# Optimization experiments

Measured on AMD Instinct MI355X. Metric: run time of the kernel, lower is better.

## Reference

```python
import jax, jax.numpy as jnp
import numpy as np

EMPTY = -1  # sentinel for empty (vertex, region) slots, as in the TF layer


def setup_inputs() -> dict:
    key = jax.random.key(0)
    m, vertices, regions = 128, 2048, 32
    # values in [-1, vertices): -1 marks an empty slot, otherwise a vertex id
    mapping = jax.random.randint(key, (m, vertices, regions), EMPTY, vertices, dtype=jnp.int32)
    return {"mapping": mapping}


def reference(mapping):
    """Faithful JAX version of Graph2Col.call.

    TF's tf.where(mask) emits coordinates of True entries in row-major order
    with a data-dependent row count. For jit-compatibility we emit a
    fixed-size [m*V*R, ...] result where valid entries come first (same
    row-major order as tf.where) and padding rows are filled with -1.
    """
    m, V, R = mapping.shape
    total = m * V * R
    flat_map = mapping.reshape(-1)                 # [total]
    # row index is never -1, so the reduce_all mask is simply mapping != -1
    flat_mask = flat_map != EMPTY                  # [total] bool

    # stable stream compaction: valid entries first, preserving row-major order
    order = jnp.argsort(~flat_mask)                # stable sort -> tf.where ordering
    valid = flat_mask[order]                       # [total] bool

    rows = order // (V * R)
    rem = order % (V * R)
    verts = rem // R
    regs = rem % R

    # column_indices: coordinates of non-empty slots (tf.where returns int64)
    column_indices = jnp.stack([rows, verts, regs], axis=-1).astype(jnp.int64)  # [total, 3]
    # nodes_indices: (batch_row, vertex_id) gathered at those coordinates (int32)
    nodes_indices = jnp.stack([rows.astype(jnp.int32), flat_map[order]], axis=-1)  # [total, 2]

    column_indices = jnp.where(valid[:, None], column_indices, jnp.int64(EMPTY))
    nodes_indices = jnp.where(valid[:, None], nodes_indices, jnp.int32(EMPTY))
    return nodes_indices, column_indices
```

## Files before the change

kernel.cpp:

```cpp
#include <hip/hip_runtime.h>


#define EMPTY_V (-1)

constexpr int M_DIM = 128;
constexpr int V_DIM = 2048;
constexpr int R_DIM = 32;
constexpr int TOTAL = M_DIM * V_DIM * R_DIM;
constexpr int BLOCK = 256;
constexpr int CHUNK = 8192;
constexpr int NB = TOTAL / CHUNK;
constexpr int SUBT = CHUNK / (BLOCK * 4);
constexpr int NWAVE = BLOCK / 64;
constexpr int STAGE = BLOCK * 4;

__global__ __launch_bounds__(BLOCK) void k_count(const int* __restrict__ in,
                                                 int* __restrict__ counts) {
    const int b = blockIdx.x;
    const int tid = threadIdx.x;
    const int4* p = (const int4*)(in + (size_t)b * CHUNK);
    int c = 0;
#pragma unroll
    for (int s = 0; s < SUBT; ++s) {
        int4 v = p[s * BLOCK + tid];
        c += (v.x != EMPTY_V) + (v.y != EMPTY_V) + (v.z != EMPTY_V) + (v.w != EMPTY_V);
    }
    for (int d = 32; d > 0; d >>= 1) c += __shfl_down(c, d, 64);
    __shared__ int ws[NWAVE];
    const int lane = tid & 63, wid = tid >> 6;
    if (lane == 0) ws[wid] = c;
    __syncthreads();
    if (tid == 0) {
        int t = 0;
        for (int w = 0; w < NWAVE; ++w) t += ws[w];
        counts[b] = t;
    }
}

__global__ __launch_bounds__(BLOCK) void k_scatter(const int* __restrict__ in,
                                                   const int* __restrict__ counts,
                                                   int* __restrict__ out_nodes,
                                                   int* __restrict__ out_cols) {
    const int b = blockIdx.x;
    const int tid = threadIdx.x;
    const int lane = tid & 63, wid = tid >> 6;
    const unsigned long long below = lane ? ((~0ull) >> (64 - lane)) : 0ull;

    __shared__ int red[2 * NWAVE];
    {
        const int4 c4 = ((const int4*)counts)[tid];
        const int idx0 = tid * 4;
        const int cs[4] = {c4.x, c4.y, c4.z, c4.w};
        int pa = 0, ta = 0;
#pragma unroll
        for (int j = 0; j < 4; ++j) {
            ta += cs[j];
            if (idx0 + j < b) pa += cs[j];
        }
        for (int d = 32; d > 0; d >>= 1) {
            pa += __shfl_down(pa, d, 64);
            ta += __shfl_down(ta, d, 64);
        }
        if (lane == 0) { red[wid] = pa; red[NWAVE + wid] = ta; }
    }
    __syncthreads();
    int running = 0, tv = 0;
    for (int w = 0; w < NWAVE; ++w) { running += red[w]; tv += red[NWAVE + w]; }

    __shared__ int wsum[NWAVE];
    __shared__ int s_val[STAGE];
    __shared__ int s_pos[STAGE];
    const int row = b >> 3;
    const int4* p = (const int4*)(in + (size_t)b * CHUNK);
#pragma unroll 1
    for (int s = 0; s < SUBT; ++s) {
        const int4 v = p[s * BLOCK + tid];
        const int f0 = (v.x != EMPTY_V), f1 = (v.y != EMPTY_V);
        const int f2 = (v.z != EMPTY_V), f3 = (v.w != EMPTY_V);
        const unsigned long long b0 = __ballot(f0), b1 = __ballot(f1);
        const unsigned long long b2 = __ballot(f2), b3 = __ballot(f3);
        const int pre = __popcll(b0 & below) + __popcll(b1 & below) +
                        __popcll(b2 & below) + __popcll(b3 & below);
        const int wtot = __popcll(b0) + __popcll(b1) + __popcll(b2) + __popcll(b3);
        if (lane == 0) wsum[wid] = wtot;
        __syncthreads();
        int woff = 0, cnt = 0;
        for (int w = 0; w < NWAVE; ++w) {
            const int x = wsum[w];
            cnt += x;
            if (w < wid) woff += x;
        }
        int lp = woff + pre;
        const int rem0 = ((b & 7) << 13) + (s << 10) + (tid << 2);
        const int vals[4] = {v.x, v.y, v.z, v.w};
        const int fl[4] = {f0, f1, f2, f3};
#pragma unroll
        for (int j = 0; j < 4; ++j) {
            if (fl[j]) { s_val[lp] = vals[j]; s_pos[lp] = rem0 + j; ++lp; }
        }
        __syncthreads();

        {
            int2* b2p = (int2*)out_nodes + running;
            const int head = ((running & 1) && cnt > 0) ? 1 : 0;
            if (head && tid == 0) b2p[0] = make_int2(row, s_val[0]);
            const int nPairs = (cnt - head) >> 1;
            int4* b4p = (int4*)(b2p + head);
            for (int k = tid; k < nPairs; k += BLOCK) {
                const int e = head + 2 * k;
                b4p[k] = make_int4(row, s_val[e], row, s_val[e + 1]);
            }
            if (((cnt - head) & 1) && tid == BLOCK - 1)
                b2p[cnt - 1] = make_int2(row, s_val[cnt - 1]);
        }
        {
            int* cd = out_cols + 3 * (size_t)running;
            const int cdw = 3 * cnt;
            const int mis = (3 * running) & 3;
            int peel = mis ? (4 - mis) : 0;
            if (peel > cdw) peel = cdw;
            if (tid < peel) {
                const int ld = tid;
                const int e = ld / 3, r = ld - 3 * e;
                int vv = row;
                if (r) { const int pp = s_pos[e]; vv = (r == 1) ? (pp >> 5) : (pp & 31); }
                cd[ld] = vv;
            }
            const int body = (cdw - peel) >> 2;
            int4* c4p = (int4*)(cd + peel);
            for (int k = tid; k < body; k += BLOCK) {
                const int ld0 = peel + 4 * k;
                int vv[4];
#pragma unroll
                for (int i = 0; i < 4; ++i) {
                    const int ld = ld0 + i;
                    const int e = ld / 3, r = ld - 3 * e;
                    int x = row;
                    if (r) { const int pp = s_pos[e]; x = (r == 1) ? (pp >> 5) : (pp & 31); }
                    vv[i] = x;
                }
                c4p[k] = make_int4(vv[0], vv[1], vv[2], vv[3]);
            }
            const int tails = cdw - peel - 4 * body;
            if (tid < tails) {
                const int ld = peel + 4 * body + tid;
                const int e = ld / 3, r = ld - 3 * e;
                int vv = row;
                if (r) { const int pp = s_pos[e]; vv = (r == 1) ? (pp >> 5) : (pp & 31); }
                cd[ld] = vv;
            }
        }
        running += cnt;
        __syncthreads();
    }

    for (int pos = tv + b * BLOCK + tid; pos < TOTAL; pos += NB * BLOCK) {
        out_nodes[2 * pos]     = EMPTY_V;
        out_nodes[2 * pos + 1] = EMPTY_V;
        out_cols[3 * pos]      = EMPTY_V;
        out_cols[3 * pos + 1]  = EMPTY_V;
        out_cols[3 * pos + 2]  = EMPTY_V;
    }
}

extern "C" void kernel_launch(void* const* d_in, const int* in_sizes, int n_in,
                              void* d_out, int out_size, void* d_ws, size_t ws_size,
                              hipStream_t stream) {
    const int* in = (const int*)d_in[0];
    int* out = (int*)d_out;
    int* out_nodes = out;
    int* out_cols = out + 2 * (size_t)TOTAL;
    int* counts = (int*)d_ws;

    k_count<<<NB, BLOCK, 0, stream>>>(in, counts);
    k_scatter<<<NB, BLOCK, 0, stream>>>(in, counts, out_nodes, out_cols);
}
```

Before: 192.0 us.

## Fuse count and scatter into single-pass decoupled look-back scan kernel

Replaces the two-kernel count-then-scatter compaction with one kernel. Each block keeps its input chunk in registers, publishes its aggregate and inclusive prefix through a status array, and resolves its exclusive offset with a warp-wide decoupled look-back. This removes the second read of the input and one kernel launch. Each block also writes its own slice of the -1 padding region, and the chunk size is doubled. In exchange it adds inter-block spinning and depends on the status buffer not holding stale flags from earlier calls, since the buffer is never cleared.

```diff
diff --git a/kernel.cpp b/kernel.cpp
--- a/kernel.cpp
+++ b/kernel.cpp
@@ -3,80 +3,98 @@
 
 #define EMPTY_V (-1)
 
-constexpr int M_DIM = 128;
-constexpr int V_DIM = 2048;
-constexpr int R_DIM = 32;
-constexpr int TOTAL = M_DIM * V_DIM * R_DIM;
+constexpr int TOTAL = 8388608;
 constexpr int BLOCK = 256;
-constexpr int CHUNK = 8192;
+constexpr int CHUNK = 16384;
 constexpr int NB = TOTAL / CHUNK;
 constexpr int SUBT = CHUNK / (BLOCK * 4);
 constexpr int NWAVE = BLOCK / 64;
 constexpr int STAGE = BLOCK * 4;
 
-__global__ __launch_bounds__(BLOCK) void k_count(const int* __restrict__ in,
-                                                 int* __restrict__ counts) {
-    const int b = blockIdx.x;
-    const int tid = threadIdx.x;
-    const int4* p = (const int4*)(in + (size_t)b * CHUNK);
-    int c = 0;
-#pragma unroll
-    for (int s = 0; s < SUBT; ++s) {
-        int4 v = p[s * BLOCK + tid];
-        c += (v.x != EMPTY_V) + (v.y != EMPTY_V) + (v.z != EMPTY_V) + (v.w != EMPTY_V);
-    }
-    for (int d = 32; d > 0; d >>= 1) c += __shfl_down(c, d, 64);
-    __shared__ int ws[NWAVE];
-    const int lane = tid & 63, wid = tid >> 6;
-    if (lane == 0) ws[wid] = c;
-    __syncthreads();
-    if (tid == 0) {
-        int t = 0;
-        for (int w = 0; w < NWAVE; ++w) t += ws[w];
-        counts[b] = t;
-    }
-}
 
-__global__ __launch_bounds__(BLOCK) void k_scatter(const int* __restrict__ in,
-                                                   const int* __restrict__ counts,
-                                                   int* __restrict__ out_nodes,
-                                                   int* __restrict__ out_cols) {
+__global__ __launch_bounds__(BLOCK, 2) void k_fused(const int* __restrict__ in,
+                                                    unsigned* __restrict__ status,
+                                                    int* __restrict__ out_nodes,
+                                                    int* __restrict__ out_cols) {
     const int b = blockIdx.x;
     const int tid = threadIdx.x;
     const int lane = tid & 63, wid = tid >> 6;
     const unsigned long long below = lane ? ((~0ull) >> (64 - lane)) : 0ull;
 
-    __shared__ int red[2 * NWAVE];
-    {
-        const int4 c4 = ((const int4*)counts)[tid];
-        const int idx0 = tid * 4;
-        const int cs[4] = {c4.x, c4.y, c4.z, c4.w};
-        int pa = 0, ta = 0;
+    int4 v[SUBT];
+    const int4* p = (const int4*)(in + (size_t)b * CHUNK);
 #pragma unroll
-        for (int j = 0; j < 4; ++j) {
-            ta += cs[j];
-            if (idx0 + j < b) pa += cs[j];
+    for (int s = 0; s < SUBT; ++s) v[s] = p[s * BLOCK + tid];
+
+    int c = 0;
+#pragma unroll
+    for (int s = 0; s < SUBT; ++s)
+        c += (v[s].x != EMPTY_V) + (v[s].y != EMPTY_V) +
+             (v[s].z != EMPTY_V) + (v[s].w != EMPTY_V);
+    for (int d = 32; d; d >>= 1) c += __shfl_down(c, d, 64);
+    __shared__ int ws[NWAVE];
+    __shared__ int s_excl;
+    if (lane == 0) ws[wid] = c;
+    __syncthreads();
+    const int agg = ws[0] + ws[1] + ws[2] + ws[3];
+
+    if (wid == 0) {
+        if (b == 0) {
+            if (lane == 0) {
+                __hip_atomic_store(&status[0], 0x20000000u | (unsigned)agg,
+                                   __ATOMIC_RELEASE, __HIP_MEMORY_SCOPE_AGENT);
+                s_excl = 0;
+            }
+        } else {
+            if (lane == 0)
+                __hip_atomic_store(&status[b], 0x10000000u | (unsigned)agg,
+                                   __ATOMIC_RELEASE, __HIP_MEMORY_SCOPE_AGENT);
+            int excl = 0, idx = b;
+            while (true) {
+                const int pb = idx - 1 - lane;
+                unsigned st;
+                if (pb >= 0) {
+                    do {
+                        st = __hip_atomic_load(&status[pb], __ATOMIC_ACQUIRE,
+                                               __HIP_MEMORY_SCOPE_AGENT);
+                    } while ((st >> 28) != 1u && (st >> 28) != 2u);
+                } else {
+                    st = 0x20000000u;
+                }
+                const unsigned fl = st >> 28;
+                int contrib = (int)(st & 0x0FFFFFFFu);
+                const unsigned long long pm = __ballot(fl == 2u);
+                if (pm) {
+                    const int Lmin = __ffsll((unsigned long long)pm) - 1;
+                    if (lane > Lmin) contrib = 0;
+                    for (int d = 32; d; d >>= 1) contrib += __shfl_down(contrib, d, 64);
+                    excl += contrib;
+                    break;
+                } else {
+                    for (int d = 32; d; d >>= 1) contrib += __shfl_down(contrib, d, 64);
+                    excl += contrib;
+                    idx -= 64;
+                }
+            }
+            if (lane == 0) {
+                __hip_atomic_store(&status[b], 0x20000000u | (unsigned)(excl + agg),
+                                   __ATOMIC_RELEASE, __HIP_MEMORY_SCOPE_AGENT);
+                s_excl = excl;
+            }
         }
-        for (int d = 32; d > 0; d >>= 1) {
-            pa += __shfl_down(pa, d, 64);
-            ta += __shfl_down(ta, d, 64);
-        }
-        if (lane == 0) { red[wid] = pa; red[NWAVE + wid] = ta; }
     }
     __syncthreads();
-    int running = 0, tv = 0;
-    for (int w = 0; w < NWAVE; ++w) { running += red[w]; tv += red[NWAVE + w]; }
+    const int excl0 = s_excl;
+    int running = excl0;
 
     __shared__ int wsum[NWAVE];
     __shared__ int s_val[STAGE];
     __shared__ int s_pos[STAGE];
-    const int row = b >> 3;
-    const int4* p = (const int4*)(in + (size_t)b * CHUNK);
-#pragma unroll 1
+    const int row = b >> 2;
+#pragma unroll
     for (int s = 0; s < SUBT; ++s) {
-        const int4 v = p[s * BLOCK + tid];
-        const int f0 = (v.x != EMPTY_V), f1 = (v.y != EMPTY_V);
-        const int f2 = (v.z != EMPTY_V), f3 = (v.w != EMPTY_V);
+        const int f0 = (v[s].x != EMPTY_V), f1 = (v[s].y != EMPTY_V);
+        const int f2 = (v[s].z != EMPTY_V), f3 = (v[s].w != EMPTY_V);
         const unsigned long long b0 = __ballot(f0), b1 = __ballot(f1);
         const unsigned long long b2 = __ballot(f2), b3 = __ballot(f3);
         const int pre = __popcll(b0 & below) + __popcll(b1 & below) +
@@ -91,12 +109,12 @@
             if (w < wid) woff += x;
         }
         int lp = woff + pre;
-        const int rem0 = ((b & 7) << 13) + (s << 10) + (tid << 2);
-        const int vals[4] = {v.x, v.y, v.z, v.w};
-        const int fl[4] = {f0, f1, f2, f3};
+        const int rem0 = ((b & 3) << 14) + (s << 10) + (tid << 2);
+        const int vals[4] = {v[s].x, v[s].y, v[s].z, v[s].w};
+        const int fl4[4] = {f0, f1, f2, f3};
 #pragma unroll
         for (int j = 0; j < 4; ++j) {
-            if (fl[j]) { s_val[lp] = vals[j]; s_pos[lp] = rem0 + j; ++lp; }
+            if (fl4[j]) { s_val[lp] = vals[j]; s_pos[lp] = rem0 + j; ++lp; }
         }
         __syncthreads();
 
@@ -154,12 +172,17 @@
         __syncthreads();
     }
 
-    for (int pos = tv + b * BLOCK + tid; pos < TOTAL; pos += NB * BLOCK) {
-        out_nodes[2 * pos]     = EMPTY_V;
-        out_nodes[2 * pos + 1] = EMPTY_V;
-        out_cols[3 * pos]      = EMPTY_V;
-        out_cols[3 * pos + 1]  = EMPTY_V;
-        out_cols[3 * pos + 2]  = EMPTY_V;
+    {
+        const int inv_pref = b * CHUNK - excl0;
+        const int start = TOTAL - inv_pref - (CHUNK - agg);
+        const int end = TOTAL - inv_pref;
+        for (int pos = start + tid; pos < end; pos += BLOCK) {
+            out_nodes[2 * pos]     = EMPTY_V;
+            out_nodes[2 * pos + 1] = EMPTY_V;
+            out_cols[3 * pos]      = EMPTY_V;
+            out_cols[3 * pos + 1]  = EMPTY_V;
+            out_cols[3 * pos + 2]  = EMPTY_V;
+        }
     }
 }
 
@@ -170,8 +193,7 @@
     int* out = (int*)d_out;
     int* out_nodes = out;
     int* out_cols = out + 2 * (size_t)TOTAL;
-    int* counts = (int*)d_ws;
+    unsigned* status = (unsigned*)d_ws;
 
-    k_count<<<NB, BLOCK, 0, stream>>>(in, counts);
-    k_scatter<<<NB, BLOCK, 0, stream>>>(in, counts, out_nodes, out_cols);
+    k_fused<<<NB, BLOCK, 0, stream>>>(in, status, out_nodes, out_cols);
 }
```

New measurement: 240.8 us. 1.25x slower.

## Stage whole chunk in LDS, single-pass compaction with swizzled staging and nontemporal stores

Applied to the files above, without the earlier changes.

The scatter kernel now uses chunks of 4096 and loads all sub-tiles up front. It computes every ballot prefix with one barrier and stages the whole chunk in LDS with an XOR swizzle, then writes the node and column outputs in one contiguous pass per block using nontemporal vector stores. This removes the per-sub-tile barriers and short write bursts of the earlier design. The padding fill is split per block by mirroring each block's invalid count into its own contiguous slice. In exchange it uses more LDS (32KB per block), which may reduce occupancy, and launches twice as many blocks, each of which reads the counts array.

```diff
diff --git a/kernel.cpp b/kernel.cpp
--- a/kernel.cpp
+++ b/kernel.cpp
@@ -3,16 +3,16 @@
 
 #define EMPTY_V (-1)
 
-constexpr int M_DIM = 128;
-constexpr int V_DIM = 2048;
-constexpr int R_DIM = 32;
-constexpr int TOTAL = M_DIM * V_DIM * R_DIM;
+typedef int v4i __attribute__((ext_vector_type(4)));
+
+constexpr int TOTAL = 8388608;
 constexpr int BLOCK = 256;
-constexpr int CHUNK = 8192;
+constexpr int CHUNK = 4096;
 constexpr int NB = TOTAL / CHUNK;
 constexpr int SUBT = CHUNK / (BLOCK * 4);
 constexpr int NWAVE = BLOCK / 64;
-constexpr int STAGE = BLOCK * 4;
+
+__device__ __forceinline__ int SW(int i) { return i ^ ((i >> 5) & 3); }
 
 __global__ __launch_bounds__(BLOCK) void k_count(const int* __restrict__ in,
                                                  int* __restrict__ counts) {
@@ -25,16 +25,12 @@
         int4 v = p[s * BLOCK + tid];
         c += (v.x != EMPTY_V) + (v.y != EMPTY_V) + (v.z != EMPTY_V) + (v.w != EMPTY_V);
     }
-    for (int d = 32; d > 0; d >>= 1) c += __shfl_down(c, d, 64);
+    for (int d = 32; d; d >>= 1) c += __shfl_down(c, d, 64);
     __shared__ int ws[NWAVE];
     const int lane = tid & 63, wid = tid >> 6;
     if (lane == 0) ws[wid] = c;
     __syncthreads();
-    if (tid == 0) {
-        int t = 0;
-        for (int w = 0; w < NWAVE; ++w) t += ws[w];
-        counts[b] = t;
-    }
+    if (tid == 0) counts[b] = ws[0] + ws[1] + ws[2] + ws[3];
 }
 
 __global__ __launch_bounds__(BLOCK) void k_scatter(const int* __restrict__ in,
@@ -46,120 +42,147 @@
     const int lane = tid & 63, wid = tid >> 6;
     const unsigned long long below = lane ? ((~0ull) >> (64 - lane)) : 0ull;
 
-    __shared__ int red[2 * NWAVE];
-    {
-        const int4 c4 = ((const int4*)counts)[tid];
-        const int idx0 = tid * 4;
-        const int cs[4] = {c4.x, c4.y, c4.z, c4.w};
+    __shared__ int red[NWAVE], redt[NWAVE];
+    __shared__ int wsum[SUBT * NWAVE];
+    __shared__ int s_val[CHUNK];
+    __shared__ int s_pos[CHUNK];
+
+    {
+        const int4 ca = ((const int4*)counts)[2 * tid];
+        const int4 cb = ((const int4*)counts)[2 * tid + 1];
+        const int idx0 = tid * 8;
+        const int cs[8] = {ca.x, ca.y, ca.z, ca.w, cb.x, cb.y, cb.z, cb.w};
         int pa = 0, ta = 0;
 #pragma unroll
-        for (int j = 0; j < 4; ++j) {
+        for (int j = 0; j < 8; ++j) {
             ta += cs[j];
             if (idx0 + j < b) pa += cs[j];
         }
-        for (int d = 32; d > 0; d >>= 1) {
+        for (int d = 32; d; d >>= 1) {
             pa += __shfl_down(pa, d, 64);
             ta += __shfl_down(ta, d, 64);
         }
-        if (lane == 0) { red[wid] = pa; red[NWAVE + wid] = ta; }
+        if (lane == 0) { red[wid] = pa; redt[wid] = ta; }
+    }
+
+    int4 v[SUBT];
+    int pre[SUBT];
+    const int4* p = (const int4*)(in + (size_t)b * CHUNK);
+#pragma unroll
+    for (int s = 0; s < SUBT; ++s) {
+        v[s] = p[s * BLOCK + tid];
+        const unsigned long long b0 = __ballot(v[s].x != EMPTY_V);
+        const unsigned long long b1 = __ballot(v[s].y != EMPTY_V);
+        const unsigned long long b2 = __ballot(v[s].z != EMPTY_V);
+        const unsigned long long b3 = __ballot(v[s].w != EMPTY_V);
+        pre[s] = __popcll(b0 & below) + __popcll(b1 & below) +
+                 __popcll(b2 & below) + __popcll(b3 & below);
+        if (lane == 0)
+            wsum[s * NWAVE + wid] =
+                __popcll(b0) + __popcll(b1) + __popcll(b2) + __popcll(b3);
     }
     __syncthreads();
-    int running = 0, tv = 0;
-    for (int w = 0; w < NWAVE; ++w) { running += red[w]; tv += red[NWAVE + w]; }
-
-    __shared__ int wsum[NWAVE];
-    __shared__ int s_val[STAGE];
-    __shared__ int s_pos[STAGE];
-    const int row = b >> 3;
-    const int4* p = (const int4*)(in + (size_t)b * CHUNK);
-#pragma unroll 1
-    for (int s = 0; s < SUBT; ++s) {
-        const int4 v = p[s * BLOCK + tid];
-        const int f0 = (v.x != EMPTY_V), f1 = (v.y != EMPTY_V);
-        const int f2 = (v.z != EMPTY_V), f3 = (v.w != EMPTY_V);
-        const unsigned long long b0 = __ballot(f0), b1 = __ballot(f1);
-        const unsigned long long b2 = __ballot(f2), b3 = __ballot(f3);
-        const int pre = __popcll(b0 & below) + __popcll(b1 & below) +
-                        __popcll(b2 & below) + __popcll(b3 & below);
-        const int wtot = __popcll(b0) + __popcll(b1) + __popcll(b2) + __popcll(b3);
-        if (lane == 0) wsum[wid] = wtot;
-        __syncthreads();
-        int woff = 0, cnt = 0;
+
+    const int excl = red[0] + red[1] + red[2] + red[3];
+    int myoff[SUBT];
+    int acc = 0;
+#pragma unroll
+    for (int s = 0; s < SUBT; ++s) {
+        int cs_ = 0, woff = 0;
+#pragma unroll
         for (int w = 0; w < NWAVE; ++w) {
-            const int x = wsum[w];
-            cnt += x;
+            const int x = wsum[s * NWAVE + w];
+            cs_ += x;
             if (w < wid) woff += x;
         }
-        int lp = woff + pre;
-        const int rem0 = ((b & 7) << 13) + (s << 10) + (tid << 2);
-        const int vals[4] = {v.x, v.y, v.z, v.w};
-        const int fl[4] = {f0, f1, f2, f3};
+        myoff[s] = acc + woff + pre[s];
+        acc += cs_;
+    }
+    const int blockValid = acc;
+
+#pragma unroll
+    for (int s = 0; s < SUBT; ++s) {
+        int lp = myoff[s];
+        const int rem0 = ((b & 15) << 12) + (s << 10) + (tid << 2);
+        const int vals[4] = {v[s].x, v[s].y, v[s].z, v[s].w};
 #pragma unroll
         for (int j = 0; j < 4; ++j) {
-            if (fl[j]) { s_val[lp] = vals[j]; s_pos[lp] = rem0 + j; ++lp; }
-        }
-        __syncthreads();
-
-        {
-            int2* b2p = (int2*)out_nodes + running;
-            const int head = ((running & 1) && cnt > 0) ? 1 : 0;
-            if (head && tid == 0) b2p[0] = make_int2(row, s_val[0]);
-            const int nPairs = (cnt - head) >> 1;
-            int4* b4p = (int4*)(b2p + head);
-            for (int k = tid; k < nPairs; k += BLOCK) {
-                const int e = head + 2 * k;
-                b4p[k] = make_int4(row, s_val[e], row, s_val[e + 1]);
+            if (vals[j] != EMPTY_V) {
+                s_val[SW(lp)] = vals[j];
+                s_pos[SW(lp)] = rem0 + j;
+                ++lp;
             }
-            if (((cnt - head) & 1) && tid == BLOCK - 1)
-                b2p[cnt - 1] = make_int2(row, s_val[cnt - 1]);
-        }
-        {
-            int* cd = out_cols + 3 * (size_t)running;
-            const int cdw = 3 * cnt;
-            const int mis = (3 * running) & 3;
-            int peel = mis ? (4 - mis) : 0;
-            if (peel > cdw) peel = cdw;
-            if (tid < peel) {
-                const int ld = tid;
+        }
+    }
+    __syncthreads();
+
+    const int row = b >> 4;
+    const int cnt = blockValid;
+
+    {
+        int2* b2p = (int2*)out_nodes + excl;
+        const int head = ((excl & 1) && cnt > 0) ? 1 : 0;
+        if (head && tid == 0) b2p[0] = make_int2(row, s_val[SW(0)]);
+        const int nPairs = (cnt - head) >> 1;
+        v4i* b4p = (v4i*)(b2p + head);
+        for (int k = tid; k < nPairs; k += BLOCK) {
+            const int e = head + 2 * k;
+            v4i t = {row, s_val[SW(e)], row, s_val[SW(e + 1)]};
+            __builtin_nontemporal_store(t, &b4p[k]);
+        }
+        if (((cnt - head) & 1) && tid == BLOCK - 1)
+            b2p[cnt - 1] = make_int2(row, s_val[SW(cnt - 1)]);
+    }
+    {
+        int* cd = out_cols + 3 * (size_t)excl;
+        const int cdw = 3 * cnt;
+        const int mis = (3 * excl) & 3;
+        int peel = mis ? (4 - mis) : 0;
+        if (peel > cdw) peel = cdw;
+        if (tid < peel) {
+            const int ld = tid;
+            const int e = ld / 3, r = ld - 3 * e;
+            int vv = row;
+            if (r) { const int pp = s_pos[SW(e)]; vv = (r == 1) ? (pp >> 5) : (pp & 31); }
+            cd[ld] = vv;
+        }
+        const int body = (cdw - peel) >> 2;
+        v4i* c4p = (v4i*)(cd + peel);
+        for (int k = tid; k < body; k += BLOCK) {
+            const int ld0 = peel + 4 * k;
+            int vv[4];
+#pragma unroll
+            for (int i = 0; i < 4; ++i) {
+                const int ld = ld0 + i;
                 const int e = ld / 3, r = ld - 3 * e;
-                int vv = row;
-                if (r) { const int pp = s_pos[e]; vv = (r == 1) ? (pp >> 5) : (pp & 31); }
-                cd[ld] = vv;
+                int x = row;
+                if (r) { const int pp = s_pos[SW(e)]; x = (r == 1) ? (pp >> 5) : (pp & 31); }
+                vv[i] = x;
             }
-            const int body = (cdw - peel) >> 2;
-            int4* c4p = (int4*)(cd + peel);
-            for (int k = tid; k < body; k += BLOCK) {
-                const int ld0 = peel + 4 * k;
-                int vv[4];
-#pragma unroll
-                for (int i = 0; i < 4; ++i) {
-                    const int ld = ld0 + i;
-                    const int e = ld / 3, r = ld - 3 * e;
-                    int x = row;
-                    if (r) { const int pp = s_pos[e]; x = (r == 1) ? (pp >> 5) : (pp & 31); }
-                    vv[i] = x;
-                }
-                c4p[k] = make_int4(vv[0], vv[1], vv[2], vv[3]);
-            }
-            const int tails = cdw - peel - 4 * body;
-            if (tid < tails) {
-                const int ld = peel + 4 * body + tid;
-                const int e = ld / 3, r = ld - 3 * e;
-                int vv = row;
-                if (r) { const int pp = s_pos[e]; vv = (r == 1) ? (pp >> 5) : (pp & 31); }
-                cd[ld] = vv;
-            }
-        }
-        running += cnt;
-        __syncthreads();
-    }
-
-    for (int pos = tv + b * BLOCK + tid; pos < TOTAL; pos += NB * BLOCK) {
-        out_nodes[2 * pos]     = EMPTY_V;
-        out_nodes[2 * pos + 1] = EMPTY_V;
-        out_cols[3 * pos]      = EMPTY_V;
-        out_cols[3 * pos + 1]  = EMPTY_V;
-        out_cols[3 * pos + 2]  = EMPTY_V;
+            v4i t = {vv[0], vv[1], vv[2], vv[3]};
+            __builtin_nontemporal_store(t, &c4p[k]);
+        }
+        const int tails = cdw - peel - 4 * body;
+        if (tid < tails) {
+            const int ld = peel + 4 * body + tid;
+            const int e = ld / 3, r = ld - 3 * e;
+            int vv = row;
+            if (r) { const int pp = s_pos[SW(e)]; vv = (r == 1) ? (pp >> 5) : (pp & 31); }
+            cd[ld] = vv;
+        }
+    }
+
+    {
+        const int inv_pref = b * CHUNK - excl;
+        const int start = TOTAL - inv_pref - (CHUNK - blockValid);
+        const int end = TOTAL - inv_pref;
+        for (int pos = start + tid; pos < end; pos += BLOCK) {
+            out_nodes[2 * pos]     = EMPTY_V;
+            out_nodes[2 * pos + 1] = EMPTY_V;
+            out_cols[3 * pos]      = EMPTY_V;
+            out_cols[3 * pos + 1]  = EMPTY_V;
+            out_cols[3 * pos + 2]  = EMPTY_V;
+        }
     }
 }
 
```

Result: slower. 200.9 us (+4.7%).
